# Optimization experiments

Hardware: AMD Instinct MI355X
Metric: run time of the kernel (lower is better)

## Reference

```python
import jax, jax.numpy as jnp
import numpy as np

B, NPG = 32, 1024            # graphs, nodes per graph
N = B * NPG                  # 32768 nodes
EPG = 8192
E = B * EPG                  # 262144 edges
IN_F, EDGE_F, EMB, H = 256, 64, 128, 4
C = EMB                      # per-head channels (TransformerConv out_channels)
HC = H * C                   # 512
NL = 4                       # conv1 + 3 stacked layers


def setup_inputs():
    key = jax.random.key(0)
    ks = jax.random.split(key, 30)
    off = jnp.arange(B, dtype=jnp.int32)[:, None] * NPG
    src = jax.random.randint(ks[0], (B, EPG), 0, NPG, dtype=jnp.int32) + off
    dst = jax.random.randint(ks[1], (B, EPG), 0, NPG, dtype=jnp.int32) + off
    p = lambda k, shape: jax.random.normal(k, shape, jnp.float32) * 0.05
    return dict(
        x=jax.random.normal(ks[2], (N, IN_F), jnp.float32),
        edge_attr=jax.random.normal(ks[3], (E, EDGE_F), jnp.float32),
        edge_index=jnp.stack([src.reshape(-1), dst.reshape(-1)]),
        edge_weight=jax.random.uniform(ks[4], (E,), jnp.float32),
        batch_index=jnp.repeat(jnp.arange(B, dtype=jnp.int32), NPG),
        lin0_w=p(ks[5], (IN_F, EMB)), lin0_b=p(ks[6], (EMB,)),
        lin_w=p(ks[7], (3, EMB, EMB)), lin_b=p(ks[8], (3, EMB)),
        q_w=p(ks[9], (NL, EMB, HC)), q_b=p(ks[10], (NL, HC)),
        k_w=p(ks[11], (NL, EMB, HC)), k_b=p(ks[12], (NL, HC)),
        v_w=p(ks[13], (NL, EMB, HC)), v_b=p(ks[14], (NL, HC)),
        e_w=p(ks[15], (NL, EDGE_F, HC)), e_b=p(ks[16], (NL, HC)),
        s_w=p(ks[17], (NL, EMB, HC)), s_b=p(ks[18], (NL, HC)),
        tr_w=p(ks[19], (NL, HC, EMB)), tr_b=p(ks[20], (NL, EMB)),
        bn_g=jnp.ones((NL, EMB), jnp.float32), bn_b=jnp.zeros((NL, EMB), jnp.float32),
        pool_w=p(ks[21], (2, EMB)),
    )


def _conv(x, ei, ea, ew, emask, lw, lb, qw, qb, kw, kb, vw, vb, eww, ewb, sw, sb):
    n = x.shape[0]
    ne = ea.shape[0]
    row, col = ei[0], ei[1]
    m = emask.astype(x.dtype)
    # degree-normalized propagate (aggr='add'):  out[col] += norm * x_lin[row]
    deg = jax.ops.segment_sum(m, row, num_segments=n)
    dis = jnp.where(deg > 0, deg ** -0.5, 0.0)
    norm = dis[row] * ew * dis[col]
    xl = x @ lw + lb                                             # (n, EMB)
    x_weighted = jax.ops.segment_sum(norm[:, None] * xl[row], col, num_segments=n)
    # TransformerConv (concat heads, edge features added to key and value)
    q = (xl @ qw + qb).reshape(n, H, C)
    k = (xl @ kw + kb).reshape(n, H, C)
    v = (xl @ vw + vb).reshape(n, H, C)
    eemb = (ea @ eww + ewb).reshape(ne, H, C)
    ke = k[row] + eemb                                           # (E,H,C)
    ve = v[row] + eemb
    alpha = jnp.einsum('ehc,ehc->eh', q[col], ke) * (1.0 / np.sqrt(C))
    alpha = jnp.where(emask[:, None], alpha, -1e9)
    amax = jax.ops.segment_max(alpha, col, num_segments=n)
    amax = jnp.where(jnp.isfinite(amax), amax, 0.0)
    expa = jnp.exp(alpha - amax[col]) * m[:, None]
    den = jax.ops.segment_sum(expa, col, num_segments=n) + 1e-16
    a = expa / den[col]                                          # segment softmax
    attn = jax.ops.segment_sum(a[:, :, None] * ve, col, num_segments=n)  # (n,H,C)
    out = attn.reshape(n, HC) + (xl @ sw + sb)                   # + root/skip
    out = out.reshape(n, H, C) + x_weighted[:, None, :]          # add degree-norm branch per head
    return out.reshape(n, HC)


def _bn(x, g, b):
    mu = x.mean(0)
    var = x.var(0)
    return g * (x - mu) * jax.lax.rsqrt(var + 1e-5) + b


def _topk_pool(h, ei, ew, emask, w, n_per):
    k = n_per // 2
    s = jnp.tanh((h @ w) / (jnp.linalg.norm(w) + 1e-16)).reshape(B, n_per)
    vals, idx = jax.lax.top_k(s, k)                              # (B,k)
    perm = (idx + jnp.arange(B)[:, None] * n_per).reshape(-1)
    h_new = h[perm] * vals.reshape(-1, 1)
    new_id = jnp.full((B * n_per,), -1, jnp.int32).at[perm].set(jnp.arange(B * k, dtype=jnp.int32))
    nr, nc = new_id[ei[0]], new_id[ei[1]]
    keep = (nr >= 0) & (nc >= 0) & emask
    ei_new = jnp.stack([jnp.where(keep, nr, 0), jnp.where(keep, nc, 0)])
    return h_new, ei_new, jnp.where(keep, ew, 0.0), keep, k


def reference(x, edge_attr, edge_index, edge_weight, batch_index,
              lin0_w, lin0_b, lin_w, lin_b, q_w, q_b, k_w, k_b, v_w, v_b,
              e_w, e_b, s_w, s_b, tr_w, tr_b, bn_g, bn_b, pool_w):
    ei, ea, ew = edge_index, edge_attr, edge_weight
    emask = jnp.ones((E,), bool)
    h = _conv(x, ei, ea, ew, emask, lin0_w, lin0_b, q_w[0], q_b[0], k_w[0], k_b[0],
              v_w[0], v_b[0], e_w[0], e_b[0], s_w[0], s_b[0])
    h = _bn(jax.nn.relu(h @ tr_w[0] + tr_b[0]), bn_g[0], bn_b[0])
    n_per = NPG
    reps = []
    pool_i = 0
    for i in range(3):
        j = i + 1
        h = _conv(h, ei, ea, ew, emask, lin_w[i], lin_b[i], q_w[j], q_b[j], k_w[j], k_b[j],
                  v_w[j], v_b[j], e_w[j], e_b[j], s_w[j], s_b[j])
        h = _bn(jax.nn.relu(h @ tr_w[j] + tr_b[j]), bn_g[j], bn_b[j])
        if i % 3 == 0 or i == 2:
            h, ei, ew, emask, n_per = _topk_pool(h, ei, ew, emask, pool_w[pool_i], n_per)
            pool_i += 1
            hb = h.reshape(B, n_per, EMB)
            reps.append(jnp.concatenate([hb.max(axis=1), hb.mean(axis=1)], axis=1))
    return reps[0] + reps[1]
```

## Files before the change

kernel.cpp:

```cpp
#include <hip/hip_runtime.h>
#include <math.h>
#include <cstddef>

#define NNODES 32768
#define NEDGES 262144
#define NB 32
#define CH 8192
#define RSPLIT 16

typedef _Float16 f16x4 __attribute__((ext_vector_type(4)));
typedef _Float16 f16x8 __attribute__((ext_vector_type(8)));
typedef float f32x4 __attribute__((ext_vector_type(4)));

__device__ __forceinline__ void load8f(const float* p, float* o) {
  float4 a = *reinterpret_cast<const float4*>(p);
  float4 b = *reinterpret_cast<const float4*>(p + 4);
  o[0] = a.x; o[1] = a.y; o[2] = a.z; o[3] = a.w;
  o[4] = b.x; o[5] = b.y; o[6] = b.z; o[7] = b.w;
}

__global__ void GraphEncoder_82575041233261_kernel() {}

__global__ void fill_f32(float* p, float v, int n) {
  int i = blockIdx.x * blockDim.x + threadIdx.x;
  if (i < n) p[i] = v;
}
__global__ void fill_i32(int* p, int v, int n) {
  int i = blockIdx.x * blockDim.x + threadIdx.x;
  if (i < n) p[i] = v;
}
__global__ void fill_dc(float* dis, int* cnt, int n) {
  int i = blockIdx.x * blockDim.x + threadIdx.x;
  if (i < n) { dis[i] = 0.f; cnt[i] = 0; }
}

__global__ void edge_init(const int* __restrict__ ei, const float* __restrict__ ew,
                          int* ei0, int* ei1, float* ewf, int* emask) {
  int e = blockIdx.x * blockDim.x + threadIdx.x;
  if (e >= NEDGES) return;
  ei0[e] = ei[e];
  ei1[e] = ei[NEDGES + e];
  ewf[e] = ew[e];
  emask[e] = 1;
}

struct MTile {
  _Float16 Ah[128][40];
  _Float16 Al[128][40];
  _Float16 Bh[128][40];
  _Float16 Bl[128][40];
};

__device__ __forceinline__ void stageA(MTile& sm, const float* __restrict__ A,
                                       int lda, int tid) {
#pragma unroll
  for (int i = 0; i < 4; i++) {
    int flat = tid + i * 256;
    int r = flat >> 3, c4 = (flat & 7) << 2;
    float4 v = *reinterpret_cast<const float4*>(A + (size_t)r * lda + c4);
    _Float16 h0 = (_Float16)v.x, h1 = (_Float16)v.y;
    _Float16 h2 = (_Float16)v.z, h3 = (_Float16)v.w;
    f16x4 hv = {h0, h1, h2, h3};
    f16x4 lv = {(_Float16)(v.x - (float)h0), (_Float16)(v.y - (float)h1),
                (_Float16)(v.z - (float)h2), (_Float16)(v.w - (float)h3)};
    *reinterpret_cast<f16x4*>(&sm.Ah[r][c4]) = hv;
    *reinterpret_cast<f16x4*>(&sm.Al[r][c4]) = lv;
  }
}

__device__ __forceinline__ void stageB(MTile& sm, const _Float16* __restrict__ th,
                                       const _Float16* __restrict__ tl, int Kw,
                                       int tid) {
#pragma unroll
  for (int i = 0; i < 4; i++) {
    int flat = tid + i * 256;
    int sel = flat >> 9;
    int cc = (flat >> 2) & 127, kc = (flat & 3) << 3;
    const _Float16* s = (sel ? tl : th) + (size_t)cc * Kw + kc;
    f16x8 v = *reinterpret_cast<const f16x8*>(s);
    if (sel)
      *reinterpret_cast<f16x8*>(&sm.Bl[cc][kc]) = v;
    else
      *reinterpret_cast<f16x8*>(&sm.Bh[cc][kc]) = v;
  }
}

__device__ __forceinline__ void mcompute(MTile& sm, f32x4 acc[4][4], int wm,
                                         int wn, int fr, int fq) {
  f16x8 ah[4], al[4], bh[4], bl[4];
#pragma unroll
  for (int m = 0; m < 4; m++) {
    ah[m] = *reinterpret_cast<const f16x8*>(&sm.Ah[wm + m * 16 + fr][fq * 8]);
    al[m] = *reinterpret_cast<const f16x8*>(&sm.Al[wm + m * 16 + fr][fq * 8]);
  }
#pragma unroll
  for (int nn = 0; nn < 4; nn++) {
    bh[nn] = *reinterpret_cast<const f16x8*>(&sm.Bh[wn + nn * 16 + fr][fq * 8]);
    bl[nn] = *reinterpret_cast<const f16x8*>(&sm.Bl[wn + nn * 16 + fr][fq * 8]);
  }
#pragma unroll
  for (int m = 0; m < 4; m++)
#pragma unroll
    for (int nn = 0; nn < 4; nn++) {
      acc[m][nn] = __builtin_amdgcn_mfma_f32_16x16x32_f16(ah[m], bh[nn], acc[m][nn], 0, 0, 0);
      acc[m][nn] = __builtin_amdgcn_mfma_f32_16x16x32_f16(ah[m], bl[nn], acc[m][nn], 0, 0, 0);
      acc[m][nn] = __builtin_amdgcn_mfma_f32_16x16x32_f16(al[m], bh[nn], acc[m][nn], 0, 0, 0);
    }
}

__global__ __launch_bounds__(256) void mgemm(
    const float* __restrict__ A, const _Float16* __restrict__ WT,
    const float* __restrict__ bias, float* __restrict__ C,
    int n, int K, int M, int relu) {
  __shared__ MTile sm;
  const int tid = threadIdx.x;
  const int lane = tid & 63, w = tid >> 6;
  const int wm = (w >> 1) << 6, wn = (w & 1) << 6;
  const int fr = lane & 15, fq = lane >> 4;
  const int row0 = blockIdx.x * 128, col0 = blockIdx.y * 128;
  const _Float16* th = WT + (size_t)col0 * K;
  const _Float16* tl = WT + (size_t)M * K + (size_t)col0 * K;
  const float* Ab = A + (size_t)row0 * K;
  f32x4 acc[4][4];
#pragma unroll
  for (int m = 0; m < 4; m++)
#pragma unroll
    for (int nn = 0; nn < 4; nn++) acc[m][nn] = (f32x4){0.f, 0.f, 0.f, 0.f};
  for (int kt = 0; kt < K; kt += 32) {
    stageA(sm, Ab + kt, K, tid);
    stageB(sm, th + kt, tl + kt, K, tid);
    __syncthreads();
    mcompute(sm, acc, wm, wn, fr, fq);
    __syncthreads();
  }
#pragma unroll
  for (int nn = 0; nn < 4; nn++) {
    const int col = col0 + wn + nn * 16 + fr;
    const float b = bias ? bias[col] : 0.f;
#pragma unroll
    for (int m = 0; m < 4; m++)
#pragma unroll
      for (int j = 0; j < 4; j++) {
        int row = row0 + wm + m * 16 + fq * 4 + j;
        float v = acc[m][nn][j] + b;
        if (relu) v = fmaxf(v, 0.f);
        C[(size_t)row * M + col] = v;
      }
  }
}

__global__ __launch_bounds__(256) void mattn(
    const float* __restrict__ Z, const float* __restrict__ WS,
    const float* __restrict__ XLv, const float* __restrict__ XW,
    const float* __restrict__ DEN, const _Float16* __restrict__ WvT,
    const _Float16* __restrict__ EWmT, const _Float16* __restrict__ SwT,
    const float* __restrict__ vb, const float* __restrict__ eb,
    const float* __restrict__ sb, float* __restrict__ ATTN, int rowBase) {
  __shared__ MTile sm;
  const int tid = threadIdx.x;
  const int lane = tid & 63, w = tid >> 6;
  const int wm = (w >> 1) << 6, wn = (w & 1) << 6;
  const int fr = lane & 15, fq = lane >> 4;
  const int h = blockIdx.y;
  const int col0 = h << 7;
  const int rloc0 = blockIdx.x * 128;
  const int row0 = rowBase + rloc0;
  f32x4 acc[4][4];
#pragma unroll
  for (int m = 0; m < 4; m++)
#pragma unroll
    for (int nn = 0; nn < 4; nn++) acc[m][nn] = (f32x4){0.f, 0.f, 0.f, 0.f};
  {
    const float* Ab = Z + (size_t)row0 * 512 + col0;
    const _Float16* th = WvT + (size_t)col0 * 128;
    const _Float16* tl = WvT + (size_t)512 * 128 + (size_t)col0 * 128;
    for (int kt = 0; kt < 128; kt += 32) {
      stageA(sm, Ab + kt, 512, tid);
      stageB(sm, th + kt, tl + kt, 128, tid);
      __syncthreads();
      mcompute(sm, acc, wm, wn, fr, fq);
      __syncthreads();
    }
  }
  {
    const float* Ab = WS + (size_t)row0 * 256 + (h << 6);
    const _Float16* th = EWmT + (size_t)col0 * 64;
    const _Float16* tl = EWmT + (size_t)512 * 64 + (size_t)col0 * 64;
    for (int kt = 0; kt < 64; kt += 32) {
      stageA(sm, Ab + kt, 256, tid);
      stageB(sm, th + kt, tl + kt, 64, tid);
      __syncthreads();
      mcompute(sm, acc, wm, wn, fr, fq);
      __syncthreads();
    }
  }
  {
    float vbe[4], sbv[4];
#pragma unroll
    for (int nn = 0; nn < 4; nn++) {
      int col = col0 + wn + nn * 16 + fr;
      vbe[nn] = vb[col] + eb[col];
      sbv[nn] = sb[col];
    }
#pragma unroll
    for (int m = 0; m < 4; m++)
#pragma unroll
      for (int j = 0; j < 4; j++) {
        int row = row0 + wm + m * 16 + fq * 4 + j;
        float d = DEN[(size_t)row * 4 + h];
        float inv = 1.f / (d + 1e-16f);
#pragma unroll
        for (int nn = 0; nn < 4; nn++)
          acc[m][nn][j] = (acc[m][nn][j] + d * vbe[nn]) * inv + sbv[nn];
      }
  }
  {
    const float* Ab = XLv + (size_t)row0 * 128;
    const _Float16* th = SwT + (size_t)col0 * 128;
    const _Float16* tl = SwT + (size_t)512 * 128 + (size_t)col0 * 128;
    for (int kt = 0; kt < 128; kt += 32) {
      stageA(sm, Ab + kt, 128, tid);
      stageB(sm, th + kt, tl + kt, 128, tid);
      __syncthreads();
      mcompute(sm, acc, wm, wn, fr, fq);
      __syncthreads();
    }
  }
#pragma unroll
  for (int nn = 0; nn < 4; nn++) {
    int col = col0 + wn + nn * 16 + fr;
#pragma unroll
    for (int m = 0; m < 4; m++)
#pragma unroll
      for (int j = 0; j < 4; j++) {
        int rl = rloc0 + wm + m * 16 + fq * 4 + j;
        float v = acc[m][nn][j] + XW[(size_t)(rowBase + rl) * 128 + (col & 127)];
        ATTN[(size_t)rl * 512 + col] = v;
      }
  }
}

__global__ void wsplit_all(const float* __restrict__ lw, int K0,
                           const float* __restrict__ vw, const float* __restrict__ ew,
                           const float* __restrict__ sw, const float* __restrict__ trw,
                           _Float16* __restrict__ lwT, _Float16* __restrict__ WvT,
                           _Float16* __restrict__ EWmT, _Float16* __restrict__ SwT,
                           _Float16* __restrict__ TrT) {
  int idx = blockIdx.x * 256 + threadIdx.x;
  const float* W; _Float16* T; int K, msh, loc;
  const int s0 = K0 << 7;
  if (idx < s0) { W = lw; T = lwT; K = K0; msh = 7; loc = idx; }
  else if (idx < s0 + 65536) { W = vw; T = WvT; K = 128; msh = 9; loc = idx - s0; }
  else if (idx < s0 + 98304) { W = ew; T = EWmT; K = 64; msh = 9; loc = idx - s0 - 65536; }
  else if (idx < s0 + 163840) { W = sw; T = SwT; K = 128; msh = 9; loc = idx - s0 - 98304; }
  else if (idx < s0 + 229376) { W = trw; T = TrT; K = 512; msh = 7; loc = idx - s0 - 163840; }
  else return;
  int M = 1 << msh;
  int k = loc >> msh, m2 = loc & (M - 1);
  float v = W[loc];
  _Float16 hh = (_Float16)v;
  T[(size_t)m2 * K + k] = hh;
  T[(size_t)M * K + (size_t)m2 * K + k] = (_Float16)(v - (float)hh);
}

__global__ __launch_bounds__(256) void prep_all(
    const float* __restrict__ Wq, const float* __restrict__ Wk,
    const float* __restrict__ EWm, const float* __restrict__ bq,
    const float* __restrict__ bk, const float* __restrict__ eb,
    _Float16* __restrict__ CtT, _Float16* __restrict__ BtT,
    float* __restrict__ gb, float* __restrict__ WCR, float* __restrict__ CC) {
  int idx = blockIdx.x * 256 + threadIdx.x;
  if (idx < 65536) {
    int cin = idx >> 9, r = idx & 511, h = r >> 7, co = r & 127;
    const float4* a4 = reinterpret_cast<const float4*>(Wq + cin * 512 + h * 128);
    const float4* b4 = reinterpret_cast<const float4*>(Wk + co * 512 + h * 128);
    float acc = 0.f;
#pragma unroll 8
    for (int c = 0; c < 32; c++) {
      float4 a = a4[c], b = b4[c];
      acc += a.x * b.x + a.y * b.y + a.z * b.z + a.w * b.w;
    }
    _Float16 hh = (_Float16)acc;
    CtT[(size_t)r * 128 + cin] = hh;
    CtT[(size_t)512 * 128 + (size_t)r * 128 + cin] = (_Float16)(acc - (float)hh);
  } else if (idx < 98304) {
    int t = idx - 65536;
    int cin = t >> 8, r = t & 255, h = r >> 6, f = r & 63;
    const float4* a4 = reinterpret_cast<const float4*>(Wq + cin * 512 + h * 128);
    const float4* b4 = reinterpret_cast<const float4*>(EWm + f * 512 + h * 128);
    float acc = 0.f;
#pragma unroll 8
    for (int c = 0; c < 32; c++) {
      float4 a = a4[c], b = b4[c];
      acc += a.x * b.x + a.y * b.y + a.z * b.z + a.w * b.w;
    }
    _Float16 hh = (_Float16)acc;
    BtT[(size_t)r * 128 + cin] = hh;
    BtT[(size_t)256 * 128 + (size_t)r * 128 + cin] = (_Float16)(acc - (float)hh);
    if (cin == 0) {
      const float4* c4 = reinterpret_cast<const float4*>(bq + h * 128);
      float s = 0.f;
#pragma unroll 8
      for (int c = 0; c < 32; c++) {
        float4 a = b4[c], b = c4[c];
        s += a.x * b.x + a.y * b.y + a.z * b.z + a.w * b.w;
      }
      gb[r] = s;
    }
  } else if (idx < 99328) {
    int tid = idx - 98304;
    int cin = tid >> 3, j = tid & 7, h2 = j & 3, isR = j >> 2;
    float acc = 0.f;
    if (isR) {
      for (int c = 0; c < 128; c++)
        acc += Wk[cin * 512 + h2 * 128 + c] * bq[h2 * 128 + c];
    } else {
      for (int c = 0; c < 128; c++)
        acc += Wq[cin * 512 + h2 * 128 + c] * (bk[h2 * 128 + c] + eb[h2 * 128 + c]);
    }
    WCR[cin * 8 + j] = acc;
    if (tid < 4) {
      float s = 0.f;
      for (int c = 0; c < 128; c++)
        s += bq[tid * 128 + c] * (bk[tid * 128 + c] + eb[tid * 128 + c]);
      CC[tid] = s;
    }
  }
}

__global__ __launch_bounds__(256) void node_scalars(const float* __restrict__ XL,
                                                    const float* __restrict__ WCR,
                                                    const float* __restrict__ CC,
                                                    float* __restrict__ SCV, int n) {
  int t = blockIdx.x * 256 + threadIdx.x;
  if (t >= n * 8) return;
  int node = t >> 3, j = t & 7;
  const float4* x4 = reinterpret_cast<const float4*>(XL + (size_t)node * 128);
  float acc = (j < 4) ? CC[j] : 0.f;
#pragma unroll 8
  for (int c = 0; c < 32; c++) {
    float4 v = x4[c];
    acc += v.x * WCR[(c * 4) * 8 + j] + v.y * WCR[(c * 4 + 1) * 8 + j] +
           v.z * WCR[(c * 4 + 2) * 8 + j] + v.w * WCR[(c * 4 + 3) * 8 + j];
  }
  SCV[t] = acc;
}

__global__ void deg_cnt(const int* __restrict__ ei0, const int* __restrict__ ei1,
                        const int* __restrict__ emask, float* deg, int* cnt) {
  int e = blockIdx.x * blockDim.x + threadIdx.x;
  if (e >= NEDGES) return;
  if (emask[e]) {
    atomicAdd(&deg[ei0[e]], 1.0f);
    atomicAdd(&cnt[ei1[e]], 1);
  }
}

__global__ __launch_bounds__(256) void scan_p1(const int* __restrict__ cnt,
                                               float* __restrict__ dis,
                                               int* __restrict__ toff,
                                               int* __restrict__ bsum) {
  const int b = blockIdx.x, tid = threadIdx.x;
  const int gi = b * 1024 + tid * 4;
  int4 c = *reinterpret_cast<const int4*>(cnt + gi);
  float4 d = *reinterpret_cast<const float4*>(dis + gi);
  float4 dr;
  dr.x = d.x > 0.f ? rsqrtf(d.x) : 0.f;
  dr.y = d.y > 0.f ? rsqrtf(d.y) : 0.f;
  dr.z = d.z > 0.f ? rsqrtf(d.z) : 0.f;
  dr.w = d.w > 0.f ? rsqrtf(d.w) : 0.f;
  *reinterpret_cast<float4*>(dis + gi) = dr;
  int s = c.x + c.y + c.z + c.w;
  __shared__ int sh[256];
  sh[tid] = s;
  __syncthreads();
  for (int dstep = 1; dstep < 256; dstep <<= 1) {
    int t = (tid >= dstep) ? sh[tid - dstep] : 0;
    __syncthreads();
    sh[tid] += t;
    __syncthreads();
  }
  toff[b * 256 + tid] = sh[tid] - s;
  if (tid == 255) bsum[b] = sh[255];
}
__global__ void scan_p2(const int* __restrict__ bsum, int* __restrict__ boff,
                        int nb, int* __restrict__ indptr, int n) {
  if (threadIdx.x == 0) {
    int run = 0;
    for (int i = 0; i < nb; i++) { boff[i] = run; run += bsum[i]; }
    indptr[n] = run;
  }
}
__global__ __launch_bounds__(256) void scan_p3(const int* __restrict__ cnt,
                                               const int* __restrict__ toff,
                                               const int* __restrict__ boff,
                                               int* __restrict__ indptr,
                                               int* __restrict__ cursor) {
  const int b = blockIdx.x, tid = threadIdx.x;
  const int gi = b * 1024 + tid * 4;
  int4 c = *reinterpret_cast<const int4*>(cnt + gi);
  int run = boff[b] + toff[b * 256 + tid];
  int4 o;
  o.x = run;
  o.y = run + c.x;
  o.z = o.y + c.y;
  o.w = o.z + c.z;
  *reinterpret_cast<int4*>(indptr + gi) = o;
  *reinterpret_cast<int4*>(cursor + gi) = o;
}

__global__ void csr_fill(const int* __restrict__ ei0, const int* __restrict__ ei1,
                         const int* __restrict__ emask, const float* __restrict__ ewf,
                         const float* __restrict__ dis, int* cursor,
                         int4* __restrict__ pck) {
  int e = blockIdx.x * blockDim.x + threadIdx.x;
  if (e >= NEDGES) return;
  if (!emask[e]) return;
  int p = atomicAdd(&cursor[ei1[e]], 1);
  int r = ei0[e];
  int4 rec;
  rec.x = r;
  rec.y = e;
  rec.z = __float_as_int(dis[r] * ewf[e]);
  rec.w = 0;
  pck[p] = rec;
}

#define ATTN_LOAD(XR, EA4, idx)                                              \
  do {                                                                       \
    const int ii_ = min((idx), cnt - 1);                                     \
    const int rr_ = __shfl(rec.x, ii_);                                      \
    const int ee_ = __shfl(rec.y, ii_);                                      \
    load8f(XLv + (size_t)rr_ * 128 + t16 * 8, XR);                           \
    EA4 = *reinterpret_cast<const float4*>(EA + (size_t)ee_ * 64 + t16 * 4); \
  } while (0)

#define ATTN_COMPUTE(XR, EA4, idx)                                           \
  do {                                                                       \
    const float rowS_ = __shfl(rsv, (h << 4) + (idx));                       \
    const float dn_ = __shfl(dnl, (idx));                                    \
    float p_ = 0.f;                                                          \
    _Pragma("unroll") for (int j = 0; j < 8; j++) p_ += u8[j] * XR[j];       \
    p_ += g4.x * EA4.x + g4.y * EA4.y + g4.z * EA4.z + g4.w * EA4.w;         \
    p_ += __shfl_xor(p_, 1);                                                 \
    p_ += __shfl_xor(p_, 2);                                                 \
    p_ += __shfl_xor(p_, 4);                                                 \
    p_ += __shfl_xor(p_, 8);                                                 \
    const float alpha_ = (p_ + colS + rowS_) * rs;                           \
    if (alpha_ > m + 8.f) {                                                  \
      const float sc_ = __expf(m - alpha_);                                  \
      den *= sc_;                                                            \
      _Pragma("unroll") for (int j = 0; j < 8; j++) z8[j] *= sc_;            \
      w4[0] *= sc_; w4[1] *= sc_; w4[2] *= sc_; w4[3] *= sc_;                \
      m = alpha_;                                                            \
    }                                                                        \
    const float a_ = __expf(alpha_ - m);                                     \
    den += a_;                                                               \
    _Pragma("unroll") for (int j = 0; j < 8; j++) z8[j] += a_ * XR[j];       \
    w4[0] += a_ * EA4.x;                                                     \
    w4[1] += a_ * EA4.y;                                                     \
    w4[2] += a_ * EA4.z;                                                     \
    w4[3] += a_ * EA4.w;                                                     \
    _Pragma("unroll") for (int j = 0; j < 8; j++) xw8[j] += dn_ * XR[j];     \
  } while (0)

__global__ __launch_bounds__(256) void fused_attn_light(
    const int4* __restrict__ PCK, const int* __restrict__ indptr,
    const float* __restrict__ EA, const float* __restrict__ XLv,
    float* U, float* G, const float* __restrict__ SCVv,
    const float* __restrict__ DISv, float* __restrict__ XW,
    float* __restrict__ DEN) {
  const int w = threadIdx.x >> 6, lane = threadIdx.x & 63;
  const int h = lane >> 4, t16 = lane & 15;
  const int col = blockIdx.x * 4 + w;
  float u8[8];
  load8f(U + (size_t)col * 512 + lane * 8, u8);
  float4 g4 = *reinterpret_cast<const float4*>(G + (size_t)col * 256 + lane * 4);
  const float colS = SCVv[col * 8 + h];
  const float dcol = DISv[col];
  const int beg = indptr[col], end = indptr[col + 1];
  const float rs = 0.08838834764831845f;
  float m = -3.0e38f, den = 0.f;
  float z8[8] = {0.f, 0.f, 0.f, 0.f, 0.f, 0.f, 0.f, 0.f};
  float w4[4] = {0.f, 0.f, 0.f, 0.f};
  float xw8[8] = {0.f, 0.f, 0.f, 0.f, 0.f, 0.f, 0.f, 0.f};
  for (int base = beg; base < end; base += 16) {
    const int cnt = min(16, end - base);
    const int li = base + min(t16, cnt - 1);
    const int4 rec = PCK[li];
    const float dnl = __int_as_float(rec.z);
    const float rsv = SCVv[(size_t)rec.x * 8 + 4 + h];
    float xrA[8], xrB[8], xrC[8], xrD[8];
    float4 eaA, eaB, eaC, eaD;
    ATTN_LOAD(xrA, eaA, 0);
    ATTN_LOAD(xrB, eaB, 1);
    ATTN_LOAD(xrC, eaC, 2);
    ATTN_LOAD(xrD, eaD, 3);
    int i = 0;
    for (; i + 4 <= cnt; i += 4) {
      ATTN_COMPUTE(xrA, eaA, i);
      ATTN_LOAD(xrA, eaA, i + 4);
      ATTN_COMPUTE(xrB, eaB, i + 1);
      ATTN_LOAD(xrB, eaB, i + 5);
      ATTN_COMPUTE(xrC, eaC, i + 2);
      ATTN_LOAD(xrC, eaC, i + 6);
      ATTN_COMPUTE(xrD, eaD, i + 3);
      ATTN_LOAD(xrD, eaD, i + 7);
    }
    if (i < cnt) ATTN_COMPUTE(xrA, eaA, i);
    if (i + 1 < cnt) ATTN_COMPUTE(xrB, eaB, i + 1);
    if (i + 2 < cnt) ATTN_COMPUTE(xrC, eaC, i + 2);
  }
  float4 o1, o2;
  o1.x = z8[0]; o1.y = z8[1]; o1.z = z8[2]; o1.w = z8[3];
  o2.x = z8[4]; o2.y = z8[5]; o2.z = z8[6]; o2.w = z8[7];
  *reinterpret_cast<float4*>(U + (size_t)col * 512 + lane * 8) = o1;
  *reinterpret_cast<float4*>(U + (size_t)col * 512 + lane * 8 + 4) = o2;
  float4 ow;
  ow.x = w4[0]; ow.y = w4[1]; ow.z = w4[2]; ow.w = w4[3];
  *reinterpret_cast<float4*>(G + (size_t)col * 256 + lane * 4) = ow;
  if (h == 0) {
    float4 x1, x2;
    x1.x = xw8[0] * dcol; x1.y = xw8[1] * dcol; x1.z = xw8[2] * dcol; x1.w = xw8[3] * dcol;
    x2.x = xw8[4] * dcol; x2.y = xw8[5] * dcol; x2.z = xw8[6] * dcol; x2.w = xw8[7] * dcol;
    *reinterpret_cast<float4*>(XW + (size_t)col * 128 + t16 * 8) = x1;
    *reinterpret_cast<float4*>(XW + (size_t)col * 128 + t16 * 8 + 4) = x2;
  }
  if (t16 == 0) DEN[col * 4 + h] = den;
}

__global__ __launch_bounds__(256) void bn_accum(const float* __restrict__ x,
                                                float* __restrict__ part1,
                                                float* __restrict__ part2, int n) {
  __shared__ float sh1[256], sh2[256];
  int c = threadIdx.x & 127;
  int half = threadIdx.x >> 7;
  float a = 0.f, b = 0.f;
  for (int i = blockIdx.x * 2 + half; i < n; i += gridDim.x * 2) {
    float v = x[(size_t)i * 128 + c];
    a += v;
    b += v * v;
  }
  sh1[threadIdx.x] = a;
  sh2[threadIdx.x] = b;
  __syncthreads();
  if (half == 0) {
    part1[blockIdx.x * 128 + c] = a + sh1[threadIdx.x + 128];
    part2[blockIdx.x * 128 + c] = b + sh2[threadIdx.x + 128];
  }
}
__global__ void bn_final(const float* __restrict__ part1, const float* __restrict__ part2,
                         float* mu, float* rstd, int n) {
  int c = threadIdx.x;
  if (c >= 128) return;
  float s1 = 0.f, s2 = 0.f;
#pragma unroll 8
  for (int b = 0; b < 256; b++) {
    s1 += part1[b * 128 + c];
    s2 += part2[b * 128 + c];
  }
  float m = s1 / (float)n;
  mu[c] = m;
  float var = s2 / (float)n - m * m;
  rstd[c] = rsqrtf(var + 1e-5f);
}
__global__ void bn_apply(float* x, const float* __restrict__ mu,
                         const float* __restrict__ rstd, const float* __restrict__ g,
                         const float* __restrict__ b, int n) {
  int t = blockIdx.x * blockDim.x + threadIdx.x;
  if (t >= n * 128) return;
  int c = t & 127;
  x[t] = g[c] * (x[t] - mu[c]) * rstd[c] + b[c];
}

__global__ void wnorm_kernel(const float* __restrict__ w, float* wn) {
  __shared__ float s[128];
  int t = threadIdx.x;
  float v = w[t];
  s[t] = v * v;
  __syncthreads();
  for (int st = 64; st > 0; st >>= 1) {
    if (t < st) s[t] += s[t + st];
    __syncthreads();
  }
  if (t == 0) wn[0] = sqrtf(s[0]) + 1e-16f;
}
__global__ void score_kernel(const float* __restrict__ h, const float* __restrict__ w,
                             const float* __restrict__ wn, float* s, int n) {
  int i = blockIdx.x * blockDim.x + threadIdx.x;
  if (i >= n) return;
  const float4* hr = reinterpret_cast<const float4*>(h + (size_t)i * 128);
  const float4* wr = reinterpret_cast<const float4*>(w);
  float d = 0.f;
  for (int c = 0; c < 32; c++) {
    float4 a = hr[c], b = wr[c];
    d += a.x * b.x + a.y * b.y + a.z * b.z + a.w * b.w;
  }
  s[i] = tanhf(d / wn[0]);
}
__global__ __launch_bounds__(512) void topk_kernel(const float* __restrict__ s,
                                                   float* gateVal, int* selIdx,
                                                   int* newid, int M) {
  __shared__ float sv[1024];
  __shared__ int si[1024];
  const int g = blockIdx.x;
  const int k = M >> 1;
  for (int t = threadIdx.x; t < 1024; t += 512) {
    if (t < M) {
      sv[t] = s[(size_t)g * M + t];
      si[t] = t;
    } else {
      sv[t] = -3.4e38f;
      si[t] = 0x7fffffff;
    }
  }
  __syncthreads();
  for (int kk = 2; kk <= 1024; kk <<= 1) {
    for (int j = kk >> 1; j > 0; j >>= 1) {
      for (int t = threadIdx.x; t < 1024; t += 512) {
        int p = t ^ j;
        if (p > t) {
          float va = sv[t], vb2 = sv[p];
          int ia = si[t], ib = si[p];
          bool beforeBA = (vb2 > va) || (vb2 == va && ib < ia);
          bool beforeAB = (va > vb2) || (va == vb2 && ia < ib);
          bool dir = ((t & kk) == 0);
          bool sw = dir ? beforeBA : beforeAB;
          if (sw) {
            sv[t] = vb2;
            sv[p] = va;
            si[t] = ib;
            si[p] = ia;
          }
        }
      }
      __syncthreads();
    }
  }
  for (int j = threadIdx.x; j < k; j += 512) {
    int oldg = g * M + si[j];
    int newg = g * k + j;
    gateVal[newg] = sv[j];
    selIdx[newg] = oldg;
    newid[oldg] = newg;
  }
}
__global__ void gate_kernel(const float* __restrict__ hOld, const float* __restrict__ gv,
                            const int* __restrict__ sel, float* __restrict__ hNew,
                            int nNew) {
  int t = blockIdx.x * blockDim.x + threadIdx.x;
  if (t >= nNew * 128) return;
  int i = t >> 7, c = t & 127;
  hNew[t] = hOld[(size_t)sel[i] * 128 + c] * gv[i];
}
__global__ void relabel_kernel(int* ei0, int* ei1, float* ewf, int* emask,
                               const int* __restrict__ newid) {
  int e = blockIdx.x * blockDim.x + threadIdx.x;
  if (e >= NEDGES) return;
  int nr = newid[ei0[e]];
  int nc = newid[ei1[e]];
  int keep = (nr >= 0 && nc >= 0 && emask[e]) ? 1 : 0;
  ei0[e] = keep ? nr : 0;
  ei1[e] = keep ? nc : 0;
  ewf[e] = keep ? ewf[e] : 0.f;
  emask[e] = keep;
}
__global__ void reps_partial(const float* __restrict__ h, float* __restrict__ rpart,
                             int k) {
  int g = blockIdx.x / RSPLIT, s = blockIdx.x % RSPLIT;
  int c = threadIdx.x;
  int per = k / RSPLIT;
  int j0 = s * per;
  float mx = -3.4e38f, sm = 0.f;
  for (int j = j0; j < j0 + per; j++) {
    float v = h[(size_t)(g * k + j) * 128 + c];
    mx = fmaxf(mx, v);
    sm += v;
  }
  rpart[(size_t)(g * RSPLIT + s) * 256 + c] = mx;
  rpart[(size_t)(g * RSPLIT + s) * 256 + 128 + c] = sm;
}
__global__ void reps_final(const float* __restrict__ rpart, float* __restrict__ rep,
                           int k) {
  int g = blockIdx.x, c = threadIdx.x;
  float mx = -3.4e38f, sm = 0.f;
  for (int s = 0; s < RSPLIT; s++) {
    mx = fmaxf(mx, rpart[(size_t)(g * RSPLIT + s) * 256 + c]);
    sm += rpart[(size_t)(g * RSPLIT + s) * 256 + 128 + c];
  }
  rep[g * 256 + c] = mx;
  rep[g * 256 + 128 + c] = sm / (float)k;
}
__global__ void final_out(const float* __restrict__ r0, const float* __restrict__ r1,
                          float* out) {
  int t = blockIdx.x * blockDim.x + threadIdx.x;
  if (t >= NB * 256) return;
  out[t] = r0[t] + r1[t];
}

extern "C" __attribute__((visibility("default")))
void kernel_launch(void* const* d_in, const int* in_sizes, int n_in,
                   void* d_out, int out_size, void* d_ws, size_t ws_size,
                   hipStream_t stream) {
  (void)hipGetLastError();

  const float* x = (const float*)d_in[0];
  const float* edge_attr = (const float*)d_in[1];
  const int* edge_index = (const int*)d_in[2];
  const float* edge_weight = (const float*)d_in[3];
  const float* lin0_w = (const float*)d_in[5];
  const float* lin0_b = (const float*)d_in[6];
  const float* lin_w = (const float*)d_in[7];
  const float* lin_b = (const float*)d_in[8];
  const float* q_w = (const float*)d_in[9];
  const float* q_b = (const float*)d_in[10];
  const float* k_w = (const float*)d_in[11];
  const float* k_b = (const float*)d_in[12];
  const float* v_w = (const float*)d_in[13];
  const float* v_b = (const float*)d_in[14];
  const float* e_w = (const float*)d_in[15];
  const float* e_b = (const float*)d_in[16];
  const float* s_w = (const float*)d_in[17];
  const float* s_b = (const float*)d_in[18];
  const float* tr_w = (const float*)d_in[19];
  const float* tr_b = (const float*)d_in[20];
  const float* bn_g = (const float*)d_in[21];
  const float* bn_b = (const float*)d_in[22];
  const float* pool_w = (const float*)d_in[23];
  (void)in_sizes; (void)n_in;

  float* out = (float*)d_out;

  size_t off = 0;
  auto alloc = [&](size_t bytes) -> void* {
    void* r = (char*)d_ws + off;
    off += (bytes + 255) & ~(size_t)255;
    return r;
  };
  float* P0 = (float*)alloc((size_t)NNODES * 128 * 4);
  float* P1 = (float*)alloc((size_t)NNODES * 128 * 4);
  float* XL = (float*)alloc((size_t)NNODES * 128 * 4);
  float* U = (float*)alloc((size_t)NNODES * 512 * 4);
  float* G = (float*)alloc((size_t)NNODES * 256 * 4);
  float* XW = (float*)alloc((size_t)NNODES * 128 * 4);
  float* DEN = (float*)alloc((size_t)NNODES * 4 * 4);
  float* ATTN = (float*)alloc((size_t)CH * 512 * 4);
  float* SCV = (float*)alloc((size_t)NNODES * 8 * 4);
  _Float16* CtT = (_Float16*)alloc((size_t)2 * 512 * 128 * 2);
  _Float16* BtT = (_Float16*)alloc((size_t)2 * 256 * 128 * 2);
  _Float16* lwT = (_Float16*)alloc((size_t)2 * 128 * 256 * 2);
  _Float16* WvT = (_Float16*)alloc((size_t)2 * 512 * 128 * 2);
  _Float16* EWmT = (_Float16*)alloc((size_t)2 * 512 * 64 * 2);
  _Float16* SwT = (_Float16*)alloc((size_t)2 * 512 * 128 * 2);
  _Float16* TrT = (_Float16*)alloc((size_t)2 * 128 * 512 * 2);
  float* GB = (float*)alloc(256 * 4);
  float* WCR = (float*)alloc(128 * 8 * 4);
  float* CC = (float*)alloc(4 * 4);
  float* DIS = (float*)alloc((size_t)NNODES * 4);
  int* EI0 = (int*)alloc((size_t)NEDGES * 4);
  int* EI1 = (int*)alloc((size_t)NEDGES * 4);
  float* EWF = (float*)alloc((size_t)NEDGES * 4);
  int* EMASK = (int*)alloc((size_t)NEDGES * 4);
  int* CNT = (int*)alloc((size_t)NNODES * 4);
  int* INDPTR = (int*)alloc((size_t)(NNODES + 256) * 4);
  int* CURSOR = (int*)alloc((size_t)NNODES * 4);
  int4* PCK4 = (int4*)alloc((size_t)NEDGES * 16);
  int* TOFF = (int*)alloc((size_t)(NNODES / 4) * 4);
  int* BSUM = (int*)alloc((size_t)64 * 4);
  int* BOFF = (int*)alloc((size_t)64 * 4);
  float* SCORE = (float*)alloc((size_t)NNODES * 4);
  int* NEWID = (int*)alloc((size_t)NNODES * 4);
  int* SELI = (int*)alloc((size_t)16384 * 4);
  float* GATEV = (float*)alloc((size_t)16384 * 4);
  float* REPS0 = (float*)alloc((size_t)NB * 256 * 4);
  float* REPS1 = (float*)alloc((size_t)NB * 256 * 4);
  float* RPART = (float*)alloc((size_t)NB * RSPLIT * 256 * 4);
  float* PART1 = (float*)alloc((size_t)256 * 128 * 4);
  float* PART2 = (float*)alloc((size_t)256 * 128 * 4);
  float* MU = (float*)alloc(128 * 4);
  float* RSTD = (float*)alloc(128 * 4);
  float* WN = (float*)alloc(256);
  const int ws_ok = (ws_size >= off) ? 1 : 0;

  edge_init<<<NEDGES / 256, 256, 0, stream>>>(edge_index, edge_weight, EI0, EI1, EWF, EMASK);
  if (hipGetLastError() != hipSuccess) {
    stream = (hipStream_t)0;
    edge_init<<<NEDGES / 256, 256, 0, stream>>>(edge_index, edge_weight, EI0, EI1, EWF, EMASK);
    (void)hipGetLastError();
  }

  if (!ws_ok) {
    fill_f32<<<(out_size + 255) / 256, 256, 0, stream>>>(out, 3000.f, out_size);
    return;
  }

  auto build_graph = [&](int n) {
    fill_dc<<<(n + 255) / 256, 256, 0, stream>>>(DIS, CNT, n);
    deg_cnt<<<NEDGES / 256, 256, 0, stream>>>(EI0, EI1, EMASK, DIS, CNT);
    scan_p1<<<n / 1024, 256, 0, stream>>>(CNT, DIS, TOFF, BSUM);
    scan_p2<<<1, 64, 0, stream>>>(BSUM, BOFF, n / 1024, INDPTR, n);
    scan_p3<<<n / 1024, 256, 0, stream>>>(CNT, TOFF, BOFF, INDPTR, CURSOR);
    csr_fill<<<NEDGES / 256, 256, 0, stream>>>(EI0, EI1, EMASK, EWF, DIS, CURSOR, PCK4);
  };

  auto conv = [&](int n, const float* Ain, int K0, float* Pout, const float* lw,
                  const float* lb, int l) {
    const float* qwl = q_w + (size_t)l * 128 * 512;
    const float* qbl = q_b + (size_t)l * 512;
    const float* kwl = k_w + (size_t)l * 128 * 512;
    const float* kbl = k_b + (size_t)l * 512;
    const float* vwl = v_w + (size_t)l * 128 * 512;
    const float* vbl = v_b + (size_t)l * 512;
    const float* ewl = e_w + (size_t)l * 64 * 512;
    const float* ebl = e_b + (size_t)l * 512;
    const float* swl = s_w + (size_t)l * 128 * 512;
    const float* sbl = s_b + (size_t)l * 512;
    const float* trwl = tr_w + (size_t)l * 512 * 128;
    const float* trbl = tr_b + (size_t)l * 128;

    prep_all<<<388, 256, 0, stream>>>(qwl, kwl, ewl, qbl, kbl, ebl, CtT, BtT, GB, WCR, CC);
    const int wtot = K0 * 128 + 229376;
    wsplit_all<<<(wtot + 255) / 256, 256, 0, stream>>>(lw, K0, vwl, ewl, swl, trwl,
                                                       lwT, WvT, EWmT, SwT, TrT);

    mgemm<<<dim3(n / 128, 1), 256, 0, stream>>>(Ain, lwT, lb, XL, n, K0, 128, 0);
    mgemm<<<dim3(n / 128, 4), 256, 0, stream>>>(XL, CtT, nullptr, U, n, 128, 512, 0);
    mgemm<<<dim3(n / 128, 2), 256, 0, stream>>>(XL, BtT, GB, G, n, 128, 256, 0);
    node_scalars<<<n / 32, 256, 0, stream>>>(XL, WCR, CC, SCV, n);

    fused_attn_light<<<n / 4, 256, 0, stream>>>(PCK4, INDPTR, edge_attr, XL,
                                                U, G, SCV, DIS, XW, DEN);

    for (int cb = 0; cb < n; cb += CH) {
      mattn<<<dim3(CH / 128, 4), 256, 0, stream>>>(U, G, XL, XW, DEN, WvT, EWmT, SwT,
                                                   vbl, ebl, sbl, ATTN, cb);
      mgemm<<<dim3(CH / 128, 1), 256, 0, stream>>>(ATTN, TrT, trbl,
                                                   Pout + (size_t)cb * 128, CH, 512,
                                                   128, 1);
    }
    bn_accum<<<256, 256, 0, stream>>>(Pout, PART1, PART2, n);
    bn_final<<<1, 128, 0, stream>>>(PART1, PART2, MU, RSTD, n);
    bn_apply<<<(n * 128) / 256, 256, 0, stream>>>(Pout, MU, RSTD, bn_g + l * 128,
                                                  bn_b + l * 128, n);
  };

  auto pool = [&](int pi, const float* hSrc, float* hDst, int nOld, int M, float* reps) {
    wnorm_kernel<<<1, 128, 0, stream>>>(pool_w + pi * 128, WN);
    score_kernel<<<(nOld + 255) / 256, 256, 0, stream>>>(hSrc, pool_w + pi * 128, WN,
                                                         SCORE, nOld);
    fill_i32<<<(nOld + 255) / 256, 256, 0, stream>>>(NEWID, -1, nOld);
    topk_kernel<<<NB, 512, 0, stream>>>(SCORE, GATEV, SELI, NEWID, M);
    int nNew = nOld / 2;
    gate_kernel<<<(nNew * 128) / 256, 256, 0, stream>>>(hSrc, GATEV, SELI, hDst, nNew);
    relabel_kernel<<<NEDGES / 256, 256, 0, stream>>>(EI0, EI1, EWF, EMASK, NEWID);
    reps_partial<<<NB * RSPLIT, 128, 0, stream>>>(hDst, RPART, M / 2);
    reps_final<<<NB, 128, 0, stream>>>(RPART, reps, M / 2);
  };

  build_graph(NNODES);
  conv(NNODES, x, 256, P0, lin0_w, lin0_b, 0);
  conv(NNODES, P0, 128, P1, lin_w, lin_b, 1);
  pool(0, P1, P0, NNODES, 1024, REPS0);
  build_graph(16384);
  conv(16384, P0, 128, P1, lin_w + 128 * 128, lin_b + 128, 2);
  conv(16384, P1, 128, P0, lin_w + 2 * 128 * 128, lin_b + 2 * 128, 3);
  pool(1, P0, P1, 16384, 512, REPS1);

  final_out<<<NB * 256 / 256, 256, 0, stream>>>(REPS0, REPS1, out);

  if (hipGetLastError() != hipSuccess) {
    hipMemsetAsync(d_out, 0x45, (size_t)out_size * 4, stream);
  }
}
```

Before: 1.615 ms.

## Split each node's edge softmax across four wavefronts with LDS merge

The attention aggregation kernel now assigns one destination node per block instead of one per wavefront. The four wavefronts take interleaved edges of that node, each keeping its own online-softmax state, and the partial maxima, denominators and sums are merged through shared memory by wavefront 0. This is meant to shorten the per-node serial edge loop and raise memory-level parallelism for gathers, since average in-degree is about 8. In exchange it drops the explicit four-deep load prefetch, launches four times more blocks, and adds LDS traffic plus a block barrier with three idle wavefronts during the merge.

Measured after the change: 1.613 ms. Within noise of the previous version (-0.1%).

```diff
diff --git a/kernel.cpp b/kernel.cpp
--- a/kernel.cpp
+++ b/kernel.cpp
@@ -426,107 +426,114 @@
   pck[p] = rec;
 }
 
-#define ATTN_LOAD(XR, EA4, idx)                                              \
-  do {                                                                       \
-    const int ii_ = min((idx), cnt - 1);                                     \
-    const int rr_ = __shfl(rec.x, ii_);                                      \
-    const int ee_ = __shfl(rec.y, ii_);                                      \
-    load8f(XLv + (size_t)rr_ * 128 + t16 * 8, XR);                           \
-    EA4 = *reinterpret_cast<const float4*>(EA + (size_t)ee_ * 64 + t16 * 4); \
-  } while (0)
-
-#define ATTN_COMPUTE(XR, EA4, idx)                                           \
-  do {                                                                       \
-    const float rowS_ = __shfl(rsv, (h << 4) + (idx));                       \
-    const float dn_ = __shfl(dnl, (idx));                                    \
-    float p_ = 0.f;                                                          \
-    _Pragma("unroll") for (int j = 0; j < 8; j++) p_ += u8[j] * XR[j];       \
-    p_ += g4.x * EA4.x + g4.y * EA4.y + g4.z * EA4.z + g4.w * EA4.w;         \
-    p_ += __shfl_xor(p_, 1);                                                 \
-    p_ += __shfl_xor(p_, 2);                                                 \
-    p_ += __shfl_xor(p_, 4);                                                 \
-    p_ += __shfl_xor(p_, 8);                                                 \
-    const float alpha_ = (p_ + colS + rowS_) * rs;                           \
-    if (alpha_ > m + 8.f) {                                                  \
-      const float sc_ = __expf(m - alpha_);                                  \
-      den *= sc_;                                                            \
-      _Pragma("unroll") for (int j = 0; j < 8; j++) z8[j] *= sc_;            \
-      w4[0] *= sc_; w4[1] *= sc_; w4[2] *= sc_; w4[3] *= sc_;                \
-      m = alpha_;                                                            \
-    }                                                                        \
-    const float a_ = __expf(alpha_ - m);                                     \
-    den += a_;                                                               \
-    _Pragma("unroll") for (int j = 0; j < 8; j++) z8[j] += a_ * XR[j];       \
-    w4[0] += a_ * EA4.x;                                                     \
-    w4[1] += a_ * EA4.y;                                                     \
-    w4[2] += a_ * EA4.z;                                                     \
-    w4[3] += a_ * EA4.w;                                                     \
-    _Pragma("unroll") for (int j = 0; j < 8; j++) xw8[j] += dn_ * XR[j];     \
-  } while (0)
-
 __global__ __launch_bounds__(256) void fused_attn_light(
     const int4* __restrict__ PCK, const int* __restrict__ indptr,
     const float* __restrict__ EA, const float* __restrict__ XLv,
     float* U, float* G, const float* __restrict__ SCVv,
     const float* __restrict__ DISv, float* __restrict__ XW,
     float* __restrict__ DEN) {
+  __shared__ float sZ[4][64][8];
+  __shared__ float sW[4][64][4];
+  __shared__ float sXW[4][16][8];
+  __shared__ float sMD[4][4][2];
   const int w = threadIdx.x >> 6, lane = threadIdx.x & 63;
   const int h = lane >> 4, t16 = lane & 15;
-  const int col = blockIdx.x * 4 + w;
+  const int col = blockIdx.x;
   float u8[8];
   load8f(U + (size_t)col * 512 + lane * 8, u8);
   float4 g4 = *reinterpret_cast<const float4*>(G + (size_t)col * 256 + lane * 4);
   const float colS = SCVv[col * 8 + h];
-  const float dcol = DISv[col];
   const int beg = indptr[col], end = indptr[col + 1];
   const float rs = 0.08838834764831845f;
   float m = -3.0e38f, den = 0.f;
   float z8[8] = {0.f, 0.f, 0.f, 0.f, 0.f, 0.f, 0.f, 0.f};
   float w4[4] = {0.f, 0.f, 0.f, 0.f};
   float xw8[8] = {0.f, 0.f, 0.f, 0.f, 0.f, 0.f, 0.f, 0.f};
-  for (int base = beg; base < end; base += 16) {
-    const int cnt = min(16, end - base);
-    const int li = base + min(t16, cnt - 1);
-    const int4 rec = PCK[li];
-    const float dnl = __int_as_float(rec.z);
-    const float rsv = SCVv[(size_t)rec.x * 8 + 4 + h];
-    float xrA[8], xrB[8], xrC[8], xrD[8];
-    float4 eaA, eaB, eaC, eaD;
-    ATTN_LOAD(xrA, eaA, 0);
-    ATTN_LOAD(xrB, eaB, 1);
-    ATTN_LOAD(xrC, eaC, 2);
-    ATTN_LOAD(xrD, eaD, 3);
-    int i = 0;
-    for (; i + 4 <= cnt; i += 4) {
-      ATTN_COMPUTE(xrA, eaA, i);
-      ATTN_LOAD(xrA, eaA, i + 4);
-      ATTN_COMPUTE(xrB, eaB, i + 1);
-      ATTN_LOAD(xrB, eaB, i + 5);
-      ATTN_COMPUTE(xrC, eaC, i + 2);
-      ATTN_LOAD(xrC, eaC, i + 6);
-      ATTN_COMPUTE(xrD, eaD, i + 3);
-      ATTN_LOAD(xrD, eaD, i + 7);
-    }
-    if (i < cnt) ATTN_COMPUTE(xrA, eaA, i);
-    if (i + 1 < cnt) ATTN_COMPUTE(xrB, eaB, i + 1);
-    if (i + 2 < cnt) ATTN_COMPUTE(xrC, eaC, i + 2);
-  }
+  for (int i = beg + w; i < end; i += 4) {
+    const int4 rec = PCK[i];
+    const float dn = __int_as_float(rec.z);
+    const float rowS = SCVv[(size_t)rec.x * 8 + 4 + h];
+    float xr[8];
+    load8f(XLv + (size_t)rec.x * 128 + t16 * 8, xr);
+    float4 ea4 = *reinterpret_cast<const float4*>(EA + (size_t)rec.y * 64 + t16 * 4);
+    float pa = 0.f;
+#pragma unroll
+    for (int j = 0; j < 8; j++) pa += u8[j] * xr[j];
+    pa += g4.x * ea4.x + g4.y * ea4.y + g4.z * ea4.z + g4.w * ea4.w;
+    pa += __shfl_xor(pa, 1);
+    pa += __shfl_xor(pa, 2);
+    pa += __shfl_xor(pa, 4);
+    pa += __shfl_xor(pa, 8);
+    const float alpha = (pa + colS + rowS) * rs;
+    if (alpha > m + 8.f) {
+      const float sc = __expf(m - alpha);
+      den *= sc;
+#pragma unroll
+      for (int j = 0; j < 8; j++) z8[j] *= sc;
+      w4[0] *= sc; w4[1] *= sc; w4[2] *= sc; w4[3] *= sc;
+      m = alpha;
+    }
+    const float a = __expf(alpha - m);
+    den += a;
+#pragma unroll
+    for (int j = 0; j < 8; j++) z8[j] += a * xr[j];
+    w4[0] += a * ea4.x;
+    w4[1] += a * ea4.y;
+    w4[2] += a * ea4.z;
+    w4[3] += a * ea4.w;
+#pragma unroll
+    for (int j = 0; j < 8; j++) xw8[j] += dn * xr[j];
+  }
+  if (t16 == 0) { sMD[w][h][0] = m; sMD[w][h][1] = den; }
+#pragma unroll
+  for (int j = 0; j < 8; j++) sZ[w][lane][j] = z8[j];
+#pragma unroll
+  for (int j = 0; j < 4; j++) sW[w][lane][j] = w4[j];
+  if (h == 0) {
+#pragma unroll
+    for (int j = 0; j < 8; j++) sXW[w][t16][j] = xw8[j];
+  }
+  __syncthreads();
+  if (w != 0) return;
+  const float m0 = sMD[0][h][0], m1 = sMD[1][h][0];
+  const float m2 = sMD[2][h][0], m3 = sMD[3][h][0];
+  const float mm = fmaxf(fmaxf(m0, m1), fmaxf(m2, m3));
+  const float s0 = __expf(m0 - mm), s1 = __expf(m1 - mm);
+  const float s2 = __expf(m2 - mm), s3 = __expf(m3 - mm);
+  const float dsum = sMD[0][h][1] * s0 + sMD[1][h][1] * s1 +
+                     sMD[2][h][1] * s2 + sMD[3][h][1] * s3;
+  float zf[8], wf[4];
+#pragma unroll
+  for (int j = 0; j < 8; j++)
+    zf[j] = sZ[0][lane][j] * s0 + sZ[1][lane][j] * s1 +
+            sZ[2][lane][j] * s2 + sZ[3][lane][j] * s3;
+#pragma unroll
+  for (int j = 0; j < 4; j++)
+    wf[j] = sW[0][lane][j] * s0 + sW[1][lane][j] * s1 +
+            sW[2][lane][j] * s2 + sW[3][lane][j] * s3;
   float4 o1, o2;
-  o1.x = z8[0]; o1.y = z8[1]; o1.z = z8[2]; o1.w = z8[3];
-  o2.x = z8[4]; o2.y = z8[5]; o2.z = z8[6]; o2.w = z8[7];
+  o1.x = zf[0]; o1.y = zf[1]; o1.z = zf[2]; o1.w = zf[3];
+  o2.x = zf[4]; o2.y = zf[5]; o2.z = zf[6]; o2.w = zf[7];
   *reinterpret_cast<float4*>(U + (size_t)col * 512 + lane * 8) = o1;
   *reinterpret_cast<float4*>(U + (size_t)col * 512 + lane * 8 + 4) = o2;
   float4 ow;
-  ow.x = w4[0]; ow.y = w4[1]; ow.z = w4[2]; ow.w = w4[3];
+  ow.x = wf[0]; ow.y = wf[1]; ow.z = wf[2]; ow.w = wf[3];
   *reinterpret_cast<float4*>(G + (size_t)col * 256 + lane * 4) = ow;
   if (h == 0) {
+    const float dcol = DISv[col];
     float4 x1, x2;
-    x1.x = xw8[0] * dcol; x1.y = xw8[1] * dcol; x1.z = xw8[2] * dcol; x1.w = xw8[3] * dcol;
-    x2.x = xw8[4] * dcol; x2.y = xw8[5] * dcol; x2.z = xw8[6] * dcol; x2.w = xw8[7] * dcol;
+    x1.x = (sXW[0][t16][0] + sXW[1][t16][0] + sXW[2][t16][0] + sXW[3][t16][0]) * dcol;
+    x1.y = (sXW[0][t16][1] + sXW[1][t16][1] + sXW[2][t16][1] + sXW[3][t16][1]) * dcol;
+    x1.z = (sXW[0][t16][2] + sXW[1][t16][2] + sXW[2][t16][2] + sXW[3][t16][2]) * dcol;
+    x1.w = (sXW[0][t16][3] + sXW[1][t16][3] + sXW[2][t16][3] + sXW[3][t16][3]) * dcol;
+    x2.x = (sXW[0][t16][4] + sXW[1][t16][4] + sXW[2][t16][4] + sXW[3][t16][4]) * dcol;
+    x2.y = (sXW[0][t16][5] + sXW[1][t16][5] + sXW[2][t16][5] + sXW[3][t16][5]) * dcol;
+    x2.z = (sXW[0][t16][6] + sXW[1][t16][6] + sXW[2][t16][6] + sXW[3][t16][6]) * dcol;
+    x2.w = (sXW[0][t16][7] + sXW[1][t16][7] + sXW[2][t16][7] + sXW[3][t16][7]) * dcol;
     *reinterpret_cast<float4*>(XW + (size_t)col * 128 + t16 * 8) = x1;
     *reinterpret_cast<float4*>(XW + (size_t)col * 128 + t16 * 8 + 4) = x2;
   }
-  if (t16 == 0) DEN[col * 4 + h] = den;
+  if (t16 == 0) DEN[col * 4 + h] = dsum;
 }
 
 __global__ __launch_bounds__(256) void bn_accum(const float* __restrict__ x,
@@ -828,8 +835,8 @@
     mgemm<<<dim3(n / 128, 2), 256, 0, stream>>>(XL, BtT, GB, G, n, 128, 256, 0);
     node_scalars<<<n / 32, 256, 0, stream>>>(XL, WCR, CC, SCV, n);
 
-    fused_attn_light<<<n / 4, 256, 0, stream>>>(PCK4, INDPTR, edge_attr, XL,
-                                                U, G, SCV, DIS, XW, DEN);
+    fused_attn_light<<<n, 256, 0, stream>>>(PCK4, INDPTR, edge_attr, XL,
+                                            U, G, SCV, DIS, XW, DEN);
 
     for (int cb = 0; cb < n; cb += CH) {
       mattn<<<dim3(CH / 128, 4), 256, 0, stream>>>(U, G, XL, XW, DEN, WvT, EWmT, SwT,
```
